# Kernel optimization log

Hardware: AMD Instinct MI355X
Metric: run time of the kernel (lower is better)

Reference implementation:

```python
import jax, jax.numpy as jnp
import numpy as np

N_NODES = 50000
N_EDGES = 600000
IN_FEATS = 128
N_HIDDEN = 128
N_CLASSES = 64


def setup_inputs() -> dict:
    key = jax.random.key(0)
    ks = jax.random.split(key, 10)
    x = jax.random.normal(ks[0], (N_NODES, IN_FEATS), dtype=jnp.float32)
    w = jax.random.uniform(ks[1], (N_EDGES,), dtype=jnp.float32)
    src = jax.random.randint(ks[2], (N_EDGES,), 0, N_NODES, dtype=jnp.int32)
    dst = jax.random.randint(ks[3], (N_EDGES,), 0, N_NODES, dtype=jnp.int32)
    W1 = jax.random.normal(ks[4], (IN_FEATS, N_HIDDEN), dtype=jnp.float32) * 0.05
    b1 = jnp.zeros((N_HIDDEN,), dtype=jnp.float32)
    W2 = jax.random.normal(ks[5], (N_HIDDEN, N_HIDDEN), dtype=jnp.float32) * 0.05
    b2 = jnp.zeros((N_HIDDEN,), dtype=jnp.float32)
    W3 = jax.random.normal(ks[6], (N_HIDDEN, N_CLASSES), dtype=jnp.float32) * 0.05
    b3 = jnp.zeros((N_CLASSES,), dtype=jnp.float32)
    return {"x": x, "w": w, "src": src, "dst": dst,
            "W1": W1, "b1": b1, "W2": W2, "b2": b2, "W3": W3, "b3": b3}


def _graph_conv(h, Wl, bl, w, src, dst, n_nodes):
    # dense linear transform
    h = h @ Wl + bl  # [N, d_out]
    # u_mul_e: gather source features, scale by edge weight
    m = h[src] * w[:, None]  # [E, d_out]
    # sum aggregation into destination nodes
    return jax.ops.segment_sum(m, dst, num_segments=n_nodes)  # [N, d_out]


def reference(x, w, src, dst, W1, b1, W2, b2, W3, b3):
    n = x.shape[0]
    h = jax.nn.relu(_graph_conv(x, W1, b1, w, src, dst, n))
    h = jax.nn.relu(_graph_conv(h, W2, b2, w, src, dst, n))
    return _graph_conv(h, W3, b3, w, src, dst, n)
```

## Files before the change

kernel.cpp:

```cpp
#include <hip/hip_runtime.h>
#include <hip/hip_fp16.h>


typedef __attribute__((ext_vector_type(8))) short short8;
typedef __attribute__((ext_vector_type(4))) float float4v;

constexpr int CAP  = 48;
constexpr int CPAD = 16;

__device__ inline unsigned bf16_rne(float f) {
    unsigned u = __float_as_uint(f);
    return (u + 0x7FFF + ((u >> 16) & 1)) >> 16;
}
__device__ inline float bf_lo(unsigned t) { return __uint_as_float(t << 16); }
__device__ inline float bf_hi(unsigned t) { return __uint_as_float(t & 0xFFFF0000u); }

__device__ inline unsigned pack_rec(int s, float wv) {
    return ((unsigned)__half_as_ushort(__float2half(wv)) << 16) | (unsigned)s;
}
__device__ inline float rec_w(unsigned r) {
    return __half2float(__ushort_as_half((unsigned short)(r >> 16)));
}
__device__ inline int rec_src(unsigned r) { return (int)(r & 0xFFFFu); }

__device__ inline void wprep_one(const float* __restrict__ Wm, int M, int tt,
                                 unsigned short* __restrict__ WfH,
                                 unsigned short* __restrict__ WfL) {
    const int FT = M / 16;
    int lane = tt & 63;
    int ft   = (tt >> 6) % FT;
    int ks   = tt / (64 * FT);
    int n     = ft * 16 + (lane & 15);
    int kbase = ks * 32 + (lane >> 4) * 8;
    #pragma unroll
    for (int j = 0; j < 8; j++) {
        float wv = Wm[(size_t)(kbase + j) * M + n];
        unsigned hb = bf16_rne(wv);
        float wh = __uint_as_float(hb << 16);
        unsigned lb = bf16_rne(wv - wh);
        WfH[(size_t)tt * 8 + j] = (unsigned short)hb;
        WfL[(size_t)tt * 8 + j] = (unsigned short)lb;
    }
}

__global__ void prep_kernel(const float* __restrict__ W1, const float* __restrict__ W2,
                            const float* __restrict__ W3,
                            unsigned short* WfH1, unsigned short* WfL1,
                            unsigned short* WfH2, unsigned short* WfL2,
                            unsigned short* WfH3, unsigned short* WfL3,
                            int* __restrict__ countsP, int N) {
    int t = blockIdx.x * blockDim.x + threadIdx.x;
    if (t < 2048)       wprep_one(W1, 128, t,        WfH1, WfL1);
    else if (t < 4096)  wprep_one(W2, 128, t - 2048, WfH2, WfL2);
    else if (t < 5120)  wprep_one(W3,  64, t - 4096, WfH3, WfL3);
    for (int i = t; i < N; i += gridDim.x * blockDim.x) countsP[i * CPAD] = 0;
}

__global__ __launch_bounds__(256) void l1_fused(
        const float* __restrict__ H,
        const unsigned short* __restrict__ WfH, const unsigned short* __restrict__ WfL,
        const float* __restrict__ bias, unsigned short* __restrict__ T,
        const int* __restrict__ src, const int* __restrict__ dst,
        const float* __restrict__ w, int* __restrict__ countsP,
        unsigned* __restrict__ erec, int N, int E, int SB) {
    const int K  = 128;
    const int KP = K + 4;
    __shared__ float Hs[32 * KP];

    if ((int)blockIdx.x < SB) {
        int e = (blockIdx.x * 256 + threadIdx.x) * 4;
        if (e + 3 < E) {
            int4   d4 = *(const int4*)(dst + e);
            int4   s4 = *(const int4*)(src + e);
            float4 w4 = *(const float4*)(w + e);
            unsigned r0 = pack_rec(s4.x, w4.x);
            unsigned r1 = pack_rec(s4.y, w4.y);
            unsigned r2 = pack_rec(s4.z, w4.z);
            unsigned r3 = pack_rec(s4.w, w4.w);
            int p0 = atomicAdd(&countsP[d4.x * CPAD], 1);
            int p1 = atomicAdd(&countsP[d4.y * CPAD], 1);
            int p2 = atomicAdd(&countsP[d4.z * CPAD], 1);
            int p3 = atomicAdd(&countsP[d4.w * CPAD], 1);
            if (p0 < CAP) erec[(size_t)d4.x * CAP + p0] = r0;
            if (p1 < CAP) erec[(size_t)d4.y * CAP + p1] = r1;
            if (p2 < CAP) erec[(size_t)d4.z * CAP + p2] = r2;
            if (p3 < CAP) erec[(size_t)d4.w * CAP + p3] = r3;
        } else {
            for (; e < E; e++) {
                int d = dst[e];
                unsigned r = pack_rec(src[e], w[e]);
                int p = atomicAdd(&countsP[d * CPAD], 1);
                if (p < CAP) erec[(size_t)d * CAP + p] = r;
            }
        }
        return;
    }

    const int node0 = (blockIdx.x - SB) * 32;
    for (int i = threadIdx.x; i < 32 * (K / 4); i += 256) {
        int r = i >> 5, c = i & 31;
        int node = node0 + r;
        float4 hv = {0, 0, 0, 0};
        if (node < N) hv = ((const float4*)(H + (size_t)node * K))[c];
        *(float4*)(Hs + r * KP + c * 4) = hv;
    }
    __syncthreads();

    const int wave = threadIdx.x >> 6;
    const int lane = threadIdx.x & 63;
    const int row  = lane & 15;
    const int ksub = (lane >> 4) * 8;
    const int rbase16 = (wave >> 1) * 16;
    const int ftbase  = (wave & 1) * 4;
    const float* hrow = Hs + (rbase16 + row) * KP;

    float4v acc[4];
    #pragma unroll
    for (int ft = 0; ft < 4; ft++) acc[ft] = (float4v){0.f, 0.f, 0.f, 0.f};

    #pragma unroll
    for (int ks = 0; ks < 4; ks++) {
        const float* ap = hrow + ks * 32 + ksub;
        float4 a0 = *(const float4*)(ap);
        float4 a1 = *(const float4*)(ap + 4);
        float av[8] = {a0.x, a0.y, a0.z, a0.w, a1.x, a1.y, a1.z, a1.w};
        short8 ah, al;
        #pragma unroll
        for (int j = 0; j < 8; j++) {
            unsigned hb = bf16_rne(av[j]);
            float fh = __uint_as_float(hb << 16);
            ah[j] = (short)hb;
            al[j] = (short)bf16_rne(av[j] - fh);
        }
        #pragma unroll
        for (int ft = 0; ft < 4; ft++) {
            int ftg = ftbase + ft;
            short8 bh = *(const short8*)(WfH + ((size_t)(ks * 8 + ftg) * 64 + lane) * 8);
            short8 bl = *(const short8*)(WfL + ((size_t)(ks * 8 + ftg) * 64 + lane) * 8);
            acc[ft] = __builtin_amdgcn_mfma_f32_16x16x32_bf16(ah, bh, acc[ft], 0, 0, 0);
            acc[ft] = __builtin_amdgcn_mfma_f32_16x16x32_bf16(al, bh, acc[ft], 0, 0, 0);
            acc[ft] = __builtin_amdgcn_mfma_f32_16x16x32_bf16(ah, bl, acc[ft], 0, 0, 0);
        }
    }

    const int col   = lane & 15;
    const int rbase = (lane >> 4) * 4;
    #pragma unroll
    for (int ft = 0; ft < 4; ft++) {
        int feat = (ftbase + ft) * 16 + col;
        float bv = bias[feat];
        #pragma unroll
        for (int r = 0; r < 4; r++) {
            int node = node0 + rbase16 + rbase + r;
            if (node < N)
                T[(size_t)node * 128 + feat] = (unsigned short)bf16_rne(acc[ft][r] + bv);
        }
    }
}

template <int MOUT>
__global__ __launch_bounds__(512) void agg_gemm(
        const unsigned short* __restrict__ Tin,
        const int* __restrict__ countsP,
        const unsigned* __restrict__ erec,
        const unsigned short* __restrict__ WfH, const unsigned short* __restrict__ WfL,
        const float* __restrict__ bias,
        unsigned short* __restrict__ T, int N) {
    constexpr int FT = MOUT / 16;
    const int wid  = threadIdx.x >> 6;
    const int lane = threadIdx.x & 63;
    __shared__ unsigned short Hsm[16][136];

    int v0 = blockIdx.x * 16 + wid * 2;
    int v0c = (v0 < N) ? v0 : N - 1;
    int v1c = (v0 + 1 < N) ? v0 + 1 : N - 1;
    const int q  = lane >> 4;
    const int fo = (lane & 15) * 8;
    const unsigned* eb0 = erec + (size_t)v0c * CAP;
    const unsigned* eb1 = erec + (size_t)v1c * CAP;

    int rx0[4], rx1[4]; float wv0[4], wv1[4];
    #pragma unroll
    for (int u = 0; u < 4; u++) {
        unsigned r0 = eb0[u * 4 + q];
        unsigned r1 = eb1[u * 4 + q];
        rx0[u] = rec_src(r0); wv0[u] = rec_w(r0);
        rx1[u] = rec_src(r1); wv1[u] = rec_w(r1);
    }
    const int c0 = min(countsP[v0c * CPAD], CAP);
    const int c1 = min(countsP[v1c * CPAD], CAP);
    const int cm = max(c0, c1);

    float A0[8] = {0, 0, 0, 0, 0, 0, 0, 0};
    float A1[8] = {0, 0, 0, 0, 0, 0, 0, 0};
    for (int i = 0; i < cm; i += 16) {
        #pragma unroll
        for (int u = 0; u < 4; u++) {
            int idx = i + u * 4 + q;
            if (idx < c0) {
                uint4 t = *(const uint4*)(Tin + (size_t)rx0[u] * 128 + fo);
                float wu = wv0[u];
                A0[0] = fmaf(wu, bf_lo(t.x), A0[0]); A0[1] = fmaf(wu, bf_hi(t.x), A0[1]);
                A0[2] = fmaf(wu, bf_lo(t.y), A0[2]); A0[3] = fmaf(wu, bf_hi(t.y), A0[3]);
                A0[4] = fmaf(wu, bf_lo(t.z), A0[4]); A0[5] = fmaf(wu, bf_hi(t.z), A0[5]);
                A0[6] = fmaf(wu, bf_lo(t.w), A0[6]); A0[7] = fmaf(wu, bf_hi(t.w), A0[7]);
            }
            if (idx < c1) {
                uint4 t = *(const uint4*)(Tin + (size_t)rx1[u] * 128 + fo);
                float wu = wv1[u];
                A1[0] = fmaf(wu, bf_lo(t.x), A1[0]); A1[1] = fmaf(wu, bf_hi(t.x), A1[1]);
                A1[2] = fmaf(wu, bf_lo(t.y), A1[2]); A1[3] = fmaf(wu, bf_hi(t.y), A1[3]);
                A1[4] = fmaf(wu, bf_lo(t.z), A1[4]); A1[5] = fmaf(wu, bf_hi(t.z), A1[5]);
                A1[6] = fmaf(wu, bf_lo(t.w), A1[6]); A1[7] = fmaf(wu, bf_hi(t.w), A1[7]);
            }
        }
        if (i + 16 < cm) {
            #pragma unroll
            for (int u = 0; u < 4; u++) {
                unsigned r0 = eb0[i + 16 + u * 4 + q];
                unsigned r1 = eb1[i + 16 + u * 4 + q];
                rx0[u] = rec_src(r0); wv0[u] = rec_w(r0);
                rx1[u] = rec_src(r1); wv1[u] = rec_w(r1);
            }
        }
    }
    #pragma unroll
    for (int j = 0; j < 8; j++) {
        A0[j] += __shfl_xor(A0[j], 32); A1[j] += __shfl_xor(A1[j], 32);
        A0[j] += __shfl_xor(A0[j], 16); A1[j] += __shfl_xor(A1[j], 16);
    }
    if (lane < 16) {
        short8 o;
        #pragma unroll
        for (int j = 0; j < 8; j++) o[j] = (short)bf16_rne(fmaxf(A0[j], 0.f));
        *(short8*)&Hsm[wid * 2][lane * 8] = o;
    } else if (lane < 32) {
        short8 o;
        #pragma unroll
        for (int j = 0; j < 8; j++) o[j] = (short)bf16_rne(fmaxf(A1[j], 0.f));
        *(short8*)&Hsm[wid * 2 + 1][(lane & 15) * 8] = o;
    }
    __syncthreads();

    if (FT == 8 || wid < FT) {
        const int ftg  = wid;
        const int row  = lane & 15;
        const int ksub = (lane >> 4) * 8;
        float4v acc = (float4v){0.f, 0.f, 0.f, 0.f};
        #pragma unroll
        for (int ks = 0; ks < 4; ks++) {
            short8 ah = *(const short8*)&Hsm[row][ks * 32 + ksub];
            short8 bh = *(const short8*)(WfH + ((size_t)(ks * FT + ftg) * 64 + lane) * 8);
            short8 bl = *(const short8*)(WfL + ((size_t)(ks * FT + ftg) * 64 + lane) * 8);
            acc = __builtin_amdgcn_mfma_f32_16x16x32_bf16(ah, bh, acc, 0, 0, 0);
            acc = __builtin_amdgcn_mfma_f32_16x16x32_bf16(ah, bl, acc, 0, 0, 0);
        }
        const int col   = lane & 15;
        const int rbase = (lane >> 4) * 4;
        const int feat  = ftg * 16 + col;
        const float bv  = bias[feat];
        #pragma unroll
        for (int r = 0; r < 4; r++) {
            int node = blockIdx.x * 16 + rbase + r;
            if (node < N)
                T[(size_t)node * MOUT + feat] = (unsigned short)bf16_rne(acc[r] + bv);
        }
    }
}

__global__ void agg_final_v4(const unsigned short* __restrict__ Tin,
                             const int* __restrict__ countsP,
                             const unsigned* __restrict__ erec,
                             float* __restrict__ OUT, int N) {
    const int wid  = threadIdx.x >> 6;
    const int lane = threadIdx.x & 63;
    const int v0 = blockIdx.x * 8 + wid * 2;
    if (v0 >= N) return;
    const int v1 = (v0 + 1 < N) ? v0 + 1 : v0;
    const int o8 = lane >> 3;
    const int fo = (lane & 7) * 8;
    const unsigned* eb0 = erec + (size_t)v0 * CAP;
    const unsigned* eb1 = erec + (size_t)v1 * CAP;

    int rx0[2], rx1[2]; float wv0[2], wv1[2];
    #pragma unroll
    for (int u = 0; u < 2; u++) {
        unsigned r0 = eb0[u * 8 + o8];
        unsigned r1 = eb1[u * 8 + o8];
        rx0[u] = rec_src(r0); wv0[u] = rec_w(r0);
        rx1[u] = rec_src(r1); wv1[u] = rec_w(r1);
    }
    const int c0 = min(countsP[v0 * CPAD], CAP);
    const int c1 = min(countsP[v1 * CPAD], CAP);
    const int cm = max(c0, c1);

    float A0[8] = {0, 0, 0, 0, 0, 0, 0, 0};
    float A1[8] = {0, 0, 0, 0, 0, 0, 0, 0};
    for (int i = 0; i < cm; i += 16) {
        #pragma unroll
        for (int u = 0; u < 2; u++) {
            int idx = i + u * 8 + o8;
            if (idx < c0) {
                uint4 t = *(const uint4*)(Tin + (size_t)rx0[u] * 64 + fo);
                float wu = wv0[u];
                A0[0] = fmaf(wu, bf_lo(t.x), A0[0]); A0[1] = fmaf(wu, bf_hi(t.x), A0[1]);
                A0[2] = fmaf(wu, bf_lo(t.y), A0[2]); A0[3] = fmaf(wu, bf_hi(t.y), A0[3]);
                A0[4] = fmaf(wu, bf_lo(t.z), A0[4]); A0[5] = fmaf(wu, bf_hi(t.z), A0[5]);
                A0[6] = fmaf(wu, bf_lo(t.w), A0[6]); A0[7] = fmaf(wu, bf_hi(t.w), A0[7]);
            }
            if (idx < c1) {
                uint4 t = *(const uint4*)(Tin + (size_t)rx1[u] * 64 + fo);
                float wu = wv1[u];
                A1[0] = fmaf(wu, bf_lo(t.x), A1[0]); A1[1] = fmaf(wu, bf_hi(t.x), A1[1]);
                A1[2] = fmaf(wu, bf_lo(t.y), A1[2]); A1[3] = fmaf(wu, bf_hi(t.y), A1[3]);
                A1[4] = fmaf(wu, bf_lo(t.z), A1[4]); A1[5] = fmaf(wu, bf_hi(t.z), A1[5]);
                A1[6] = fmaf(wu, bf_lo(t.w), A1[6]); A1[7] = fmaf(wu, bf_hi(t.w), A1[7]);
            }
        }
        if (i + 16 < cm) {
            #pragma unroll
            for (int u = 0; u < 2; u++) {
                unsigned r0 = eb0[i + 16 + u * 8 + o8];
                unsigned r1 = eb1[i + 16 + u * 8 + o8];
                rx0[u] = rec_src(r0); wv0[u] = rec_w(r0);
                rx1[u] = rec_src(r1); wv1[u] = rec_w(r1);
            }
        }
    }
    #pragma unroll
    for (int j = 0; j < 8; j++) {
        A0[j] += __shfl_xor(A0[j], 32); A1[j] += __shfl_xor(A1[j], 32);
        A0[j] += __shfl_xor(A0[j], 16); A1[j] += __shfl_xor(A1[j], 16);
        A0[j] += __shfl_xor(A0[j], 8);  A1[j] += __shfl_xor(A1[j], 8);
    }
    if (lane < 8) {
        float4 o0 = {A0[0], A0[1], A0[2], A0[3]};
        float4 o1 = {A0[4], A0[5], A0[6], A0[7]};
        float* op = OUT + (size_t)v0 * 64 + fo;
        *(float4*)(op)     = o0;
        *(float4*)(op + 4) = o1;
    } else if (lane < 16 && v1 != v0) {
        float4 o0 = {A1[0], A1[1], A1[2], A1[3]};
        float4 o1 = {A1[4], A1[5], A1[6], A1[7]};
        float* op = OUT + (size_t)v1 * 64 + fo;
        *(float4*)(op)     = o0;
        *(float4*)(op + 4) = o1;
    }
}

extern "C" void kernel_launch(void* const* d_in, const int* in_sizes, int n_in,
                              void* d_out, int out_size, void* d_ws, size_t ws_size,
                              hipStream_t stream) {
    const float* x   = (const float*)d_in[0];
    const float* w   = (const float*)d_in[1];
    const int*   src = (const int*)d_in[2];
    const int*   dst = (const int*)d_in[3];
    const float* W1  = (const float*)d_in[4];
    const float* b1  = (const float*)d_in[5];
    const float* W2  = (const float*)d_in[6];
    const float* b2  = (const float*)d_in[7];
    const float* W3  = (const float*)d_in[8];
    const float* b3  = (const float*)d_in[9];
    const int N = in_sizes[0] / 128;
    const int E = in_sizes[1];

    unsigned short* Ta   = (unsigned short*)d_ws;
    unsigned short* Tb   = Ta + (size_t)N * 128;
    unsigned* erec = (unsigned*)(Tb + (size_t)N * 128);
    int*  countsP  = (int*)(erec + (size_t)N * CAP);
    size_t coff = (size_t)((char*)(countsP + (size_t)N * CPAD) - (char*)d_ws);
    coff = (coff + 15) & ~(size_t)15;
    unsigned short* WfH1 = (unsigned short*)((char*)d_ws + coff);
    unsigned short* WfL1 = WfH1 + 128 * 128;
    unsigned short* WfH2 = WfL1 + 128 * 128;
    unsigned short* WfL2 = WfH2 + 128 * 128;
    unsigned short* WfH3 = WfL2 + 128 * 128;
    unsigned short* WfL3 = WfH3 + 128 * 64;

    const int GB  = (N + 31) / 32;
    const int SB  = (E / 4 + 255) / 256;
    const int AGB = (N + 15) / 16;
    const int AB  = (N + 7) / 8;

    prep_kernel<<<96, 256, 0, stream>>>(W1, W2, W3, WfH1, WfL1, WfH2, WfL2,
                                        WfH3, WfL3, countsP, N);
    l1_fused<<<SB + GB, 256, 0, stream>>>(x, WfH1, WfL1, b1, Ta,
                                          src, dst, w, countsP, erec, N, E, SB);
    agg_gemm<128><<<AGB, 512, 0, stream>>>(Ta, countsP, erec, WfH2, WfL2, b2, Tb, N);
    agg_gemm<64><<<AGB, 512, 0, stream>>>(Tb, countsP, erec, WfH3, WfL3, b3, Ta, N);
    agg_final_v4<<<AB, 256, 0, stream>>>(Ta, countsP, erec, (float*)d_out, N);
}
```

Before: 215.1 us.

## Split final-layer features into two planar halves, aggregating each half separately

The third-layer GEMM now writes its bf16 output in a planar layout of two 32-feature slabs (feature-half major, then node). The final aggregation kernel launches twice as many blocks, each covering one half, and gathers 64-byte rows instead of 128-byte rows. The aim is to shrink the gather working set per pass so it stays resident in cache, and to raise parallelism. In exchange, edge records and counts are read twice and the loop overhead per feature doubles.

```diff
diff --git a/kernel.cpp b/kernel.cpp
--- a/kernel.cpp
+++ b/kernel.cpp
@@ -158,7 +158,7 @@
     }
 }
 
-template <int MOUT>
+template <int MOUT, bool PLANAR>
 __global__ __launch_bounds__(512) void agg_gemm(
         const unsigned short* __restrict__ Tin,
         const int* __restrict__ countsP,
@@ -262,23 +262,31 @@
         #pragma unroll
         for (int r = 0; r < 4; r++) {
             int node = blockIdx.x * 16 + rbase + r;
-            if (node < N)
-                T[(size_t)node * MOUT + feat] = (unsigned short)bf16_rne(acc[r] + bv);
-        }
-    }
-}
-
-__global__ void agg_final_v4(const unsigned short* __restrict__ Tin,
+            if (node < N) {
+                unsigned short val = (unsigned short)bf16_rne(acc[r] + bv);
+                if (PLANAR)
+                    T[((size_t)(feat >> 5) * N + node) * 32 + (feat & 31)] = val;
+                else
+                    T[(size_t)node * MOUT + feat] = val;
+            }
+        }
+    }
+}
+
+__global__ void agg_final_v5(const unsigned short* __restrict__ Tin,
                              const int* __restrict__ countsP,
                              const unsigned* __restrict__ erec,
-                             float* __restrict__ OUT, int N) {
+                             float* __restrict__ OUT, int N, int AB) {
+    const int half = ((int)blockIdx.x >= AB) ? 1 : 0;
+    const int vblk = (int)blockIdx.x - half * AB;
     const int wid  = threadIdx.x >> 6;
     const int lane = threadIdx.x & 63;
-    const int v0 = blockIdx.x * 8 + wid * 2;
+    const int v0 = vblk * 8 + wid * 2;
     if (v0 >= N) return;
     const int v1 = (v0 + 1 < N) ? v0 + 1 : v0;
     const int o8 = lane >> 3;
-    const int fo = (lane & 7) * 8;
+    const int fo = (lane & 7) * 4;
+    const unsigned short* Tp = Tin + (size_t)half * N * 32;
     const unsigned* eb0 = erec + (size_t)v0 * CAP;
     const unsigned* eb1 = erec + (size_t)v1 * CAP;
 
@@ -294,27 +302,23 @@
     const int c1 = min(countsP[v1 * CPAD], CAP);
     const int cm = max(c0, c1);
 
-    float A0[8] = {0, 0, 0, 0, 0, 0, 0, 0};
-    float A1[8] = {0, 0, 0, 0, 0, 0, 0, 0};
+    float A0[4] = {0, 0, 0, 0};
+    float A1[4] = {0, 0, 0, 0};
     for (int i = 0; i < cm; i += 16) {
         #pragma unroll
         for (int u = 0; u < 2; u++) {
             int idx = i + u * 8 + o8;
             if (idx < c0) {
-                uint4 t = *(const uint4*)(Tin + (size_t)rx0[u] * 64 + fo);
+                uint2 t = *(const uint2*)(Tp + (size_t)rx0[u] * 32 + fo);
                 float wu = wv0[u];
                 A0[0] = fmaf(wu, bf_lo(t.x), A0[0]); A0[1] = fmaf(wu, bf_hi(t.x), A0[1]);
                 A0[2] = fmaf(wu, bf_lo(t.y), A0[2]); A0[3] = fmaf(wu, bf_hi(t.y), A0[3]);
-                A0[4] = fmaf(wu, bf_lo(t.z), A0[4]); A0[5] = fmaf(wu, bf_hi(t.z), A0[5]);
-                A0[6] = fmaf(wu, bf_lo(t.w), A0[6]); A0[7] = fmaf(wu, bf_hi(t.w), A0[7]);
             }
             if (idx < c1) {
-                uint4 t = *(const uint4*)(Tin + (size_t)rx1[u] * 64 + fo);
+                uint2 t = *(const uint2*)(Tp + (size_t)rx1[u] * 32 + fo);
                 float wu = wv1[u];
                 A1[0] = fmaf(wu, bf_lo(t.x), A1[0]); A1[1] = fmaf(wu, bf_hi(t.x), A1[1]);
                 A1[2] = fmaf(wu, bf_lo(t.y), A1[2]); A1[3] = fmaf(wu, bf_hi(t.y), A1[3]);
-                A1[4] = fmaf(wu, bf_lo(t.z), A1[4]); A1[5] = fmaf(wu, bf_hi(t.z), A1[5]);
-                A1[6] = fmaf(wu, bf_lo(t.w), A1[6]); A1[7] = fmaf(wu, bf_hi(t.w), A1[7]);
             }
         }
         if (i + 16 < cm) {
@@ -328,23 +332,17 @@
         }
     }
     #pragma unroll
-    for (int j = 0; j < 8; j++) {
+    for (int j = 0; j < 4; j++) {
         A0[j] += __shfl_xor(A0[j], 32); A1[j] += __shfl_xor(A1[j], 32);
         A0[j] += __shfl_xor(A0[j], 16); A1[j] += __shfl_xor(A1[j], 16);
         A0[j] += __shfl_xor(A0[j], 8);  A1[j] += __shfl_xor(A1[j], 8);
     }
     if (lane < 8) {
         float4 o0 = {A0[0], A0[1], A0[2], A0[3]};
-        float4 o1 = {A0[4], A0[5], A0[6], A0[7]};
-        float* op = OUT + (size_t)v0 * 64 + fo;
-        *(float4*)(op)     = o0;
-        *(float4*)(op + 4) = o1;
+        *(float4*)(OUT + (size_t)v0 * 64 + half * 32 + fo) = o0;
     } else if (lane < 16 && v1 != v0) {
         float4 o0 = {A1[0], A1[1], A1[2], A1[3]};
-        float4 o1 = {A1[4], A1[5], A1[6], A1[7]};
-        float* op = OUT + (size_t)v1 * 64 + fo;
-        *(float4*)(op)     = o0;
-        *(float4*)(op + 4) = o1;
+        *(float4*)(OUT + (size_t)v1 * 64 + half * 32 + fo) = o0;
     }
 }
 
@@ -386,7 +384,10 @@
                                         WfH3, WfL3, countsP, N);
     l1_fused<<<SB + GB, 256, 0, stream>>>(x, WfH1, WfL1, b1, Ta,
                                           src, dst, w, countsP, erec, N, E, SB);
-    agg_gemm<128><<<AGB, 512, 0, stream>>>(Ta, countsP, erec, WfH2, WfL2, b2, Tb, N);
-    agg_gemm<64><<<AGB, 512, 0, stream>>>(Tb, countsP, erec, WfH3, WfL3, b3, Ta, N);
-    agg_final_v4<<<AB, 256, 0, stream>>>(Ta, countsP, erec, (float*)d_out, N);
-}
+    agg_gemm<128, false><<<AGB, 512, 0, stream>>>(Ta, countsP, erec,
+                                                  WfH2, WfL2, b2, Tb, N);
+    agg_gemm<64, true><<<AGB, 512, 0, stream>>>(Tb, countsP, erec,
+                                                WfH3, WfL3, b3, Ta, N);
+    agg_final_v5<<<2 * AB, 256, 0, stream>>>(Ta, countsP, erec,
+                                             (float*)d_out, N, AB);
+}
```

Measured after the change: 222.5 us. 3.4% more time.
